# Kernel tuning notes

Hardware: AMD Instinct MI355X
Metric: run time of the kernel (lower is better)

## Reference

```python
import jax, jax.numpy as jnp
import numpy as np

ELEM, EMBD = 512, 512

def setup_inputs() -> dict:
    key = jax.random.key(0)
    ks = jax.random.split(key, 7)
    s = 1.0 / np.sqrt(ELEM)
    return {
        "x": jax.random.normal(ks[0], (8, 2048, ELEM), dtype=jnp.float32),
        "Wq": jax.random.normal(ks[1], (ELEM, EMBD), dtype=jnp.float32) * s,
        "bq": jnp.zeros((EMBD,), dtype=jnp.float32),
        "Wk": jax.random.normal(ks[2], (ELEM, EMBD), dtype=jnp.float32) * s,
        "bk": jnp.zeros((EMBD,), dtype=jnp.float32),
        "Wv": jax.random.normal(ks[3], (ELEM, EMBD), dtype=jnp.float32) * s,
        "bv": jnp.zeros((EMBD,), dtype=jnp.float32),
    }

def reference(x, Wq, bq, Wk, bk, Wv, bv):
    # x: [N, S, E]
    q = x @ Wq + bq            # [N, S, D]
    k = x @ Wk + bk            # [N, S, D]
    v = x @ Wv + bv            # [N, S, D]
    # NOTE: original has no 1/sqrt(d) scaling.
    logits = jnp.einsum('nsd,ntd->nst', q, k)   # [N, S, S]
    attn = jax.nn.softmax(logits, axis=-1)
    return jnp.einsum('nst,ntd->nsd', attn, v)  # [N, S, D]
```

## Files before the change

kernel.cpp:

```cpp
#include <hip/hip_runtime.h>
#include <hip/hip_fp16.h>

#define SEQ 2048
#define DIM 512

typedef __attribute__((ext_vector_type(8))) short short8;
typedef __attribute__((ext_vector_type(4))) float f32x4;
typedef _Float16 h8 __attribute__((ext_vector_type(8)));
typedef _Float16 h4 __attribute__((ext_vector_type(4)));

#define MFMA16(a, b, c) __builtin_amdgcn_mfma_f32_16x16x32_f16((a), (b), (c), 0, 0, 0)

#define GLOAD_LDS16(g, l)                                                              \
    __builtin_amdgcn_global_load_lds(                                                  \
        (const __attribute__((address_space(1))) unsigned int*)(g),                    \
        (__attribute__((address_space(3))) unsigned int*)(l), 16, 0, 0)

template <int MODE>
__global__ __launch_bounds__(256) void gemmc(
    const _Float16* __restrict__ A, const _Float16* __restrict__ B,
    const float* __restrict__ bq, const float* __restrict__ bk,
    const float* __restrict__ bv,
    _Float16* __restrict__ oq, _Float16* __restrict__ ok, _Float16* __restrict__ ovt,
    float* __restrict__ of, int bat0) {
    __shared__ char sm[3 * 16384];
    constexpr int T  = (MODE == 0) ? 32 : (MODE == 1) ? 16 : 64;
    constexpr int PA = (MODE == 0) ? 512 : (MODE == 1) ? 512 : 4096;
    constexpr int PB = (MODE == 0) ? 1024 : (MODE == 1) ? 512 : 2048;

    int tid = threadIdx.x, wid = tid >> 6, lane = tid & 63, r = lane & 15, g = lane >> 4;
    int mw = wid >> 1, nw = wid & 1;
    int m0 = blockIdx.x * 128, n0 = blockIdx.y * 128, bz = blockIdx.z;

    const _Float16 *Ab, *Bb;
    if (MODE == 0) {
        Ab = A + (size_t)m0 * 512;
        Bb = B + (size_t)n0 * 1024;
    } else if (MODE == 1) {
        int b = bat0 + bz;
        Ab = A + ((size_t)(b * SEQ) + m0) * 512;
        Bb = B + ((size_t)(b * SEQ) + n0) * 512;
    } else {
        int b = bat0 + bz;
        Ab = A + (size_t)bz * (SEQ * 4096) + (size_t)m0 * 4096;
        Bb = B + (size_t)b * (512 * SEQ) + (size_t)n0 * 2048;
    }

    const char* gA[2];
    const char* gB[2];
    int ldsw[2];
#pragma unroll
    for (int j = 0; j < 2; ++j) {
        int c = (j * 4 + wid) * 64 + lane;
        int row = c >> 2, s = c & 3;
        int col16 = s ^ ((row >> 1) & 3);
        gA[j] = (const char*)Ab + (size_t)row * (PA * 2) + col16 * 16;
        gB[j] = (const char*)Bb + (size_t)row * (PB * 2) + col16 * 16;
        ldsw[j] = (j * 4 + wid) * 1024;
    }
    int offA[4], offB[4];
#pragma unroll
    for (int m = 0; m < 4; ++m) {
        int rowA = mw * 64 + m * 16 + r;
        offA[m] = rowA * 64 + ((g ^ ((rowA >> 1) & 3)) * 16);
        int rowB = nw * 64 + m * 16 + r;
        offB[m] = rowB * 64 + ((g ^ ((rowB >> 1) & 3)) * 16);
    }

    f32x4 acc[4][4];
#pragma unroll
    for (int m = 0; m < 4; ++m)
#pragma unroll
        for (int n = 0; n < 4; ++n) acc[m][n] = (f32x4)(0.0f);

    auto STG = [&](int t, int b) {
        int ka = (MODE == 0) ? ((t & 15) * 64) : (t * 64);
        int kb = t * 64;
        char* dA = sm + b * 16384;
        char* dB = sm + b * 16384 + 8192;
        GLOAD_LDS16(gA[0] + ka, dA + ldsw[0]);
        GLOAD_LDS16(gA[1] + ka, dA + ldsw[1]);
        GLOAD_LDS16(gB[0] + kb, dB + ldsw[0]);
        GLOAD_LDS16(gB[1] + kb, dB + ldsw[1]);
    };

    STG(0, 0);
    STG(1, 1);
    asm volatile("s_waitcnt vmcnt(4)" ::: "memory");
    __builtin_amdgcn_s_barrier();

#pragma unroll
    for (int t = 0; t < T; ++t) {
        const int buf = t % 3;
        if (t + 2 < T) STG(t + 2, (t + 2) % 3);
        const char* bA = sm + buf * 16384;
        const char* bB = sm + buf * 16384 + 8192;
        h8 af[4], bf[4];
#pragma unroll
        for (int m = 0; m < 4; ++m) af[m] = *(const h8*)(bA + offA[m]);
#pragma unroll
        for (int n = 0; n < 4; ++n) bf[n] = *(const h8*)(bB + offB[n]);
#pragma unroll
        for (int m = 0; m < 4; ++m)
#pragma unroll
            for (int n = 0; n < 4; ++n)
                acc[m][n] = MFMA16(af[m], bf[n], acc[m][n]);
        if (t + 2 < T) asm volatile("s_waitcnt vmcnt(4)" ::: "memory");
        else if (t + 1 < T) asm volatile("s_waitcnt vmcnt(0)" ::: "memory");
        if (t + 1 < T) __builtin_amdgcn_s_barrier();
    }

    if (MODE == 0) {
        int p = n0 >> 9;
        int ncl = n0 & 511;
        const float* bias = (p == 0) ? bq : (p == 1) ? bk : bv;
#pragma unroll
        for (int n = 0; n < 4; ++n) {
            int col = ncl + nw * 64 + n * 16 + r;
            float bi = bias[col];
#pragma unroll
            for (int m = 0; m < 4; ++m) {
                int grow0 = m0 + mw * 64 + m * 16 + 4 * g;
                if (p == 0) {
                    for (int reg = 0; reg < 4; ++reg)
                        oq[(size_t)(grow0 + reg) * 512 + col] =
                            (_Float16)(acc[m][n][reg] + bi);
                } else if (p == 1) {
                    for (int reg = 0; reg < 4; ++reg)
                        ok[(size_t)(grow0 + reg) * 512 + col] =
                            (_Float16)(acc[m][n][reg] + bi);
                } else {
                    int b = grow0 >> 11, s0 = grow0 & 2047;
                    h4 pv;
                    pv[0] = (_Float16)(acc[m][n][0] + bi);
                    pv[1] = (_Float16)(acc[m][n][1] + bi);
                    pv[2] = (_Float16)(acc[m][n][2] + bi);
                    pv[3] = (_Float16)(acc[m][n][3] + bi);
                    *(h4*)(&ovt[(size_t)b * (512 * 2048) + (size_t)col * 2048 + s0]) = pv;
                }
            }
        }
    } else if (MODE == 1) {
        float* sb = of + (size_t)bz * (SEQ * (size_t)SEQ);
#pragma unroll
        for (int n = 0; n < 4; ++n) {
            int col = n0 + nw * 64 + n * 16 + r;
#pragma unroll
            for (int m = 0; m < 4; ++m) {
                int grow0 = m0 + mw * 64 + m * 16 + 4 * g;
                for (int reg = 0; reg < 4; ++reg)
                    sb[(size_t)(grow0 + reg) * SEQ + col] = acc[m][n][reg];
            }
        }
    } else {
        int b = bat0 + bz;
#pragma unroll
        for (int n = 0; n < 4; ++n) {
            int col = n0 + nw * 64 + n * 16 + r;
#pragma unroll
            for (int m = 0; m < 4; ++m) {
                int grow0 = m0 + mw * 64 + m * 16 + 4 * g;
                for (int reg = 0; reg < 4; ++reg)
                    of[(size_t)(b * SEQ + grow0 + reg) * 512 + col] = acc[m][n][reg];
            }
        }
    }
}

__global__ __launch_bounds__(256) void k0a_splitw(
    const float* __restrict__ Wq, const float* __restrict__ Wk, const float* __restrict__ Wv,
    _Float16* __restrict__ wstk) {
    int idx = blockIdx.x * 256 + threadIdx.x;
    int p = idx >> 18;
    int rem = idx & 262143;
    int k = rem >> 9, n = rem & 511;
    const float* W = (p == 0) ? Wq : (p == 1) ? Wk : Wv;
    float w = W[rem];
    _Float16 h = (_Float16)w;
    size_t base = (size_t)(p * 512 + n) * 1024;
    wstk[base + k] = h;
    wstk[base + 512 + k] = (_Float16)(w - (float)h);
}

__global__ __launch_bounds__(256) void k0b_splitx(
    const float* __restrict__ x, _Float16* __restrict__ xh) {
    size_t i = (size_t)(blockIdx.x * 256 + threadIdx.x) * 4;
    float4 v = *(const float4*)(x + i);
    h4 h;
    h[0] = (_Float16)v.x; h[1] = (_Float16)v.y;
    h[2] = (_Float16)v.z; h[3] = (_Float16)v.w;
    *(h4*)(xh + i) = h;
}

__global__ __launch_bounds__(256) void k3_softmax(float* __restrict__ sbuf) {
    size_t row = blockIdx.x;
    float* srow = sbuf + row * SEQ;
    int tid = threadIdx.x, lane = tid & 63, wid = tid >> 6;
    float4 v0 = *(const float4*)(srow + tid * 8);
    float4 v1 = *(const float4*)(srow + tid * 8 + 4);
    float m = fmaxf(fmaxf(fmaxf(v0.x, v0.y), fmaxf(v0.z, v0.w)),
                    fmaxf(fmaxf(v1.x, v1.y), fmaxf(v1.z, v1.w)));
    for (int d = 1; d < 64; d <<= 1) m = fmaxf(m, __shfl_xor(m, d));
    __shared__ float red1[4], red2[4];
    if (lane == 0) red1[wid] = m;
    __syncthreads();
    m = fmaxf(fmaxf(red1[0], red1[1]), fmaxf(red1[2], red1[3]));
    float e[8];
    e[0] = __expf(v0.x - m); e[1] = __expf(v0.y - m);
    e[2] = __expf(v0.z - m); e[3] = __expf(v0.w - m);
    e[4] = __expf(v1.x - m); e[5] = __expf(v1.y - m);
    e[6] = __expf(v1.z - m); e[7] = __expf(v1.w - m);
    float s = ((e[0] + e[1]) + (e[2] + e[3])) + ((e[4] + e[5]) + (e[6] + e[7]));
    for (int d = 1; d < 64; d <<= 1) s += __shfl_xor(s, d);
    if (lane == 0) red2[wid] = s;
    __syncthreads();
    s = (red2[0] + red2[1]) + (red2[2] + red2[3]);
    float inv = 1.0f / s;
    h8 ph;
    for (int j = 0; j < 8; ++j) ph[j] = (_Float16)(e[j] * inv);
    *(h8*)((char*)srow + (size_t)tid * 16) = ph;
}

extern "C" void kernel_launch(void* const* d_in, const int* in_sizes, int n_in,
                              void* d_out, int out_size, void* d_ws, size_t ws_size,
                              hipStream_t stream) {
    const float* x  = (const float*)d_in[0];
    const float* Wq = (const float*)d_in[1];
    const float* bq = (const float*)d_in[2];
    const float* Wk = (const float*)d_in[3];
    const float* bk = (const float*)d_in[4];
    const float* Wv = (const float*)d_in[5];
    const float* bv = (const float*)d_in[6];
    float* out = (float*)d_out;

    char* ws = (char*)d_ws;
    const size_t QSZ = 16777216;
    _Float16* wstk = (_Float16*)(ws);
    _Float16* xh = (_Float16*)(ws + 3145728);
    _Float16* qh = (_Float16*)(ws + 3145728 + 1 * QSZ);
    _Float16* kh = (_Float16*)(ws + 3145728 + 2 * QSZ);
    _Float16* vt = (_Float16*)(ws + 3145728 + 3 * QSZ);
    const size_t sbase = 3145728 + 4 * QSZ;

    k0a_splitw<<<3072, 256, 0, stream>>>(Wq, Wk, Wv, wstk);
    k0b_splitx<<<8192, 256, 0, stream>>>(x, xh);
    gemmc<0><<<dim3(128, 12), 256, 0, stream>>>(xh, wstk, bq, bk, bv,
                                                qh, kh, vt, nullptr, 0);

    size_t avail = (ws_size > sbase) ? (ws_size - sbase) : 0;
    int chunk = (int)(avail / QSZ);
    if (chunk < 1) chunk = 1;
    if (chunk > 8) chunk = 8;
    float* sc = (float*)(ws + sbase);
    for (int b0 = 0; b0 < 8; b0 += chunk) {
        int nb = (8 - b0 < chunk) ? (8 - b0) : chunk;
        gemmc<1><<<dim3(16, 16, nb), 256, 0, stream>>>(qh, kh, nullptr, nullptr, nullptr,
                                                       nullptr, nullptr, nullptr, sc, b0);
        k3_softmax<<<dim3(nb * SEQ), 256, 0, stream>>>(sc);
        gemmc<2><<<dim3(16, 4, nb), 256, 0, stream>>>((const _Float16*)sc, vt,
                                                      nullptr, nullptr, nullptr,
                                                      nullptr, nullptr, nullptr, out, b0);
    }
}
```

Measured before the change: 210.1 us.

## Use 128-wide K tiles with double buffering in the fp16 GEMM kernel

Widens each K stage from 64 to 128 elements, so there are half as many loop iterations and barriers. Shared-memory buffering moves from three 16KB stages to two 32KB stages, with a new 8-way XOR swizzle for the wider rows. Each stage now runs 32 MFMAs per barrier instead of 16, which cuts synchronisation overhead. In exchange, prefetch depth drops to one stage and the loop waits for vmcnt(0) every iteration, which may expose more load latency. LDS use also rises to 64KB, which could lower occupancy.

```diff
diff --git a/kernel.cpp b/kernel.cpp
--- a/kernel.cpp
+++ b/kernel.cpp
@@ -23,8 +23,8 @@
     const float* __restrict__ bv,
     _Float16* __restrict__ oq, _Float16* __restrict__ ok, _Float16* __restrict__ ovt,
     float* __restrict__ of, int bat0) {
-    __shared__ char sm[3 * 16384];
-    constexpr int T  = (MODE == 0) ? 32 : (MODE == 1) ? 16 : 64;
+    __shared__ char sm[2 * 32768];
+    constexpr int T  = (MODE == 0) ? 16 : (MODE == 1) ? 8 : 32;
     constexpr int PA = (MODE == 0) ? 512 : (MODE == 1) ? 512 : 4096;
     constexpr int PB = (MODE == 0) ? 1024 : (MODE == 1) ? 512 : 2048;
 
@@ -46,25 +46,28 @@
         Bb = B + (size_t)b * (512 * SEQ) + (size_t)n0 * 2048;
     }
 
-    const char* gA[2];
-    const char* gB[2];
-    int ldsw[2];
-#pragma unroll
-    for (int j = 0; j < 2; ++j) {
-        int c = (j * 4 + wid) * 64 + lane;
-        int row = c >> 2, s = c & 3;
-        int col16 = s ^ ((row >> 1) & 3);
+    const char* gA[4];
+    const char* gB[4];
+    int ldsw[4];
+#pragma unroll
+    for (int j = 0; j < 4; ++j) {
+        int ci = (j * 4 + wid) * 64 + lane;
+        int row = ci >> 3, cl = ci & 7;
+        int col16 = cl ^ (row & 7);
         gA[j] = (const char*)Ab + (size_t)row * (PA * 2) + col16 * 16;
         gB[j] = (const char*)Bb + (size_t)row * (PB * 2) + col16 * 16;
         ldsw[j] = (j * 4 + wid) * 1024;
     }
-    int offA[4], offB[4];
+    int offA[4][2], offB[4][2];
 #pragma unroll
     for (int m = 0; m < 4; ++m) {
         int rowA = mw * 64 + m * 16 + r;
-        offA[m] = rowA * 64 + ((g ^ ((rowA >> 1) & 3)) * 16);
         int rowB = nw * 64 + m * 16 + r;
-        offB[m] = rowB * 64 + ((g ^ ((rowB >> 1) & 3)) * 16);
+#pragma unroll
+        for (int ks = 0; ks < 2; ++ks) {
+            offA[m][ks] = rowA * 128 + (((ks * 4 + g) ^ (rowA & 7)) * 16);
+            offB[m][ks] = rowB * 128 + (((ks * 4 + g) ^ (rowB & 7)) * 16);
+        }
     }
 
     f32x4 acc[4][4];
@@ -74,40 +77,46 @@
         for (int n = 0; n < 4; ++n) acc[m][n] = (f32x4)(0.0f);
 
     auto STG = [&](int t, int b) {
-        int ka = (MODE == 0) ? ((t & 15) * 64) : (t * 64);
-        int kb = t * 64;
-        char* dA = sm + b * 16384;
-        char* dB = sm + b * 16384 + 8192;
-        GLOAD_LDS16(gA[0] + ka, dA + ldsw[0]);
-        GLOAD_LDS16(gA[1] + ka, dA + ldsw[1]);
-        GLOAD_LDS16(gB[0] + kb, dB + ldsw[0]);
-        GLOAD_LDS16(gB[1] + kb, dB + ldsw[1]);
+        int ka = (MODE == 0) ? ((t & 7) * 128) : (t * 128);
+        int kb = t * 128;
+        char* dA = sm + b * 32768;
+        char* dB = sm + b * 32768 + 16384;
+#pragma unroll
+        for (int j = 0; j < 4; ++j) {
+            GLOAD_LDS16(gA[j] + ka, dA + ldsw[j]);
+            GLOAD_LDS16(gB[j] + kb, dB + ldsw[j]);
+        }
     };
 
     STG(0, 0);
-    STG(1, 1);
-    asm volatile("s_waitcnt vmcnt(4)" ::: "memory");
+    asm volatile("s_waitcnt vmcnt(0)" ::: "memory");
     __builtin_amdgcn_s_barrier();
 
 #pragma unroll
     for (int t = 0; t < T; ++t) {
-        const int buf = t % 3;
-        if (t + 2 < T) STG(t + 2, (t + 2) % 3);
-        const char* bA = sm + buf * 16384;
-        const char* bB = sm + buf * 16384 + 8192;
-        h8 af[4], bf[4];
-#pragma unroll
-        for (int m = 0; m < 4; ++m) af[m] = *(const h8*)(bA + offA[m]);
-#pragma unroll
-        for (int n = 0; n < 4; ++n) bf[n] = *(const h8*)(bB + offB[n]);
+        const int buf = t & 1;
+        if (t + 1 < T) STG(t + 1, buf ^ 1);
+        const char* bA = sm + buf * 32768;
+        const char* bB = sm + buf * 32768 + 16384;
+        h8 af[4][2], bf[4][2];
 #pragma unroll
         for (int m = 0; m < 4; ++m)
 #pragma unroll
-            for (int n = 0; n < 4; ++n)
-                acc[m][n] = MFMA16(af[m], bf[n], acc[m][n]);
-        if (t + 2 < T) asm volatile("s_waitcnt vmcnt(4)" ::: "memory");
-        else if (t + 1 < T) asm volatile("s_waitcnt vmcnt(0)" ::: "memory");
-        if (t + 1 < T) __builtin_amdgcn_s_barrier();
+            for (int ks = 0; ks < 2; ++ks) {
+                af[m][ks] = *(const h8*)(bA + offA[m][ks]);
+                bf[m][ks] = *(const h8*)(bB + offB[m][ks]);
+            }
+#pragma unroll
+        for (int ks = 0; ks < 2; ++ks)
+#pragma unroll
+            for (int m = 0; m < 4; ++m)
+#pragma unroll
+                for (int n = 0; n < 4; ++n)
+                    acc[m][n] = MFMA16(af[m][ks], bf[n][ks], acc[m][n]);
+        if (t + 1 < T) {
+            asm volatile("s_waitcnt vmcnt(0)" ::: "memory");
+            __builtin_amdgcn_s_barrier();
+        }
     }
 
     if (MODE == 0) {
```

Result: faster. 189.1 us (-10.0%).
